# Performance work log

Hardware: AMD Instinct MI355X
Metric: run time of the kernel (lower is better)

Reference implementation:

```python
import jax, jax.numpy as jnp
import numpy as np

EMBED_DIM = 1024
HIDDEN_DIM = 1024
NUM_HEADS = 16
CONTEXT_DIM = 768
HEAD_DIM = EMBED_DIM // NUM_HEADS
SCALE = HEAD_DIM ** -0.5


def setup_inputs() -> dict:
    key = jax.random.key(0)
    ks = jax.random.split(key, 7)
    B, N, M = 4, 4096, 1024
    tokens = jax.random.normal(ks[0], (B, N, HIDDEN_DIM), dtype=jnp.float32)
    context = jax.random.normal(ks[1], (B, M, CONTEXT_DIM), dtype=jnp.float32)
    # Linear weights stored as [in, out] (transposed torch layout)
    Wq = jax.random.normal(ks[2], (HIDDEN_DIM, EMBED_DIM), dtype=jnp.float32) * (HIDDEN_DIM ** -0.5)
    Wk = jax.random.normal(ks[3], (CONTEXT_DIM, EMBED_DIM), dtype=jnp.float32) * (CONTEXT_DIM ** -0.5)
    Wv = jax.random.normal(ks[4], (CONTEXT_DIM, HIDDEN_DIM), dtype=jnp.float32) * (CONTEXT_DIM ** -0.5)
    Wo = jax.random.normal(ks[5], (HIDDEN_DIM, HIDDEN_DIM), dtype=jnp.float32) * (HIDDEN_DIM ** -0.5)
    bo = jax.random.normal(ks[6], (HIDDEN_DIM,), dtype=jnp.float32) * 0.01
    return {"tokens": tokens, "context": context, "Wq": Wq, "Wk": Wk, "Wv": Wv, "Wo": Wo, "bo": bo}


def _split_heads(x):
    # [b, n, h*d] -> [b, h, n, d]
    b, n, _ = x.shape
    return x.reshape(b, n, NUM_HEADS, -1).transpose(0, 2, 1, 3)


def reference(tokens, context, Wq, Wk, Wv, Wo, bo):
    Q = _split_heads(tokens @ Wq)    # [b, h, n, d]
    K = _split_heads(context @ Wk)   # [b, h, m, d]
    V = _split_heads(context @ Wv)   # [b, h, m, dv]
    scores = jnp.einsum('bhnd,bhmd->bhnm', Q, K) * SCALE
    attn = jax.nn.softmax(scores, axis=-1)
    out = jnp.einsum('bhnm,bhmd->bhnd', attn, V)          # [b, h, n, dv]
    b, h, n, d = out.shape
    out = out.transpose(0, 2, 1, 3).reshape(b, n, h * d)  # [b, n, hidden]
    return out @ Wo + bo
```

## Files before the change

### kernel.cpp

```cpp
#include <hip/hip_runtime.h>
#include <hip/hip_bf16.h>
#include <math.h>

typedef unsigned short ushort_t;
typedef __attribute__((ext_vector_type(8))) short short8;
typedef __attribute__((ext_vector_type(4))) short short4v;
typedef __attribute__((ext_vector_type(4))) float f32x4;

#define MFMA16(a, b, c) __builtin_amdgcn_mfma_f32_16x16x32_bf16((a), (b), (c), 0, 0, 0)

__device__ __forceinline__ short8 ld_s8(const void* p) { return *(const short8*)p; }

__device__ __forceinline__ ushort_t f2bf(float x) {
  __hip_bfloat16 h = __float2bfloat16(x);
  return *reinterpret_cast<ushort_t*>(&h);
}

__device__ __forceinline__ void wave_fence() {
  __builtin_amdgcn_fence(__ATOMIC_ACQ_REL, "wavefront");
}

__device__ __forceinline__ void async_ld16(const void* g, void* l) {
  __builtin_amdgcn_global_load_lds(
      (const __attribute__((address_space(1))) unsigned int*)g,
      (__attribute__((address_space(3))) unsigned int*)l, 16, 0, 0);
}

__global__ __launch_bounds__(256) void cvt_k(const float* __restrict__ src,
                                             ushort_t* __restrict__ dst, size_t n8) {
  const size_t i = (size_t)blockIdx.x * 256 + threadIdx.x;
  if (i >= n8) return;
  const size_t base = i * 8;
  const float4 a = ((const float4*)(src + base))[0];
  const float4 b = ((const float4*)(src + base))[1];
  short8 o;
  o[0] = (short)f2bf(a.x); o[1] = (short)f2bf(a.y);
  o[2] = (short)f2bf(a.z); o[3] = (short)f2bf(a.w);
  o[4] = (short)f2bf(b.x); o[5] = (short)f2bf(b.y);
  o[6] = (short)f2bf(b.z); o[7] = (short)f2bf(b.w);
  *(short8*)(dst + base) = o;
}

__global__ void transpose_cvt2_k(const float* __restrict__ s0, const float* __restrict__ s1,
                                 ushort_t* __restrict__ d0, ushort_t* __restrict__ d1,
                                 int R, int C) {
  __shared__ ushort_t tile[32][33];
  const float* src = blockIdx.z ? s1 : s0;
  ushort_t* dst = blockIdx.z ? d1 : d0;
  const int bx = blockIdx.x * 32, by = blockIdx.y * 32;
  const int tx = threadIdx.x, ty = threadIdx.y;
#pragma unroll
  for (int i = 0; i < 32; i += 8)
    tile[ty + i][tx] = f2bf(src[(size_t)(by + ty + i) * C + bx + tx]);
  __syncthreads();
#pragma unroll
  for (int i = 0; i < 32; i += 8)
    dst[(size_t)(bx + ty + i) * R + by + tx] = tile[tx][ty + i];
}

#define BM 128
#define BN 128
#define BK 32

__device__ __forceinline__ void st1(float* p, float v) { *p = v; }
__device__ __forceinline__ void st1(__hip_bfloat16* p, float v) { *p = __float2bfloat16(v); }

__device__ __forceinline__ int2 xcd_swz(int nx) {
  const int id = blockIdx.y * gridDim.x + blockIdx.x;
  const int cpx = (gridDim.x * gridDim.y) >> 3;
  const int nid = (id & 7) * cpx + (id >> 3);
  int2 r; r.x = nid % nx; r.y = nid / nx; return r;
}

#define GSTAGE(sA, sB)                                          \
  do {                                                          \
    async_ld16(Ag + (size_t)srow * K + (k0 + scol), (sA) + wb); \
    async_ld16(Ag + (size_t)(srow + 64) * K + (k0 + scol), (sA) + 2048 + wb); \
    async_ld16(Bg + (size_t)srow * K + (k0 + scol), (sB) + wb); \
    async_ld16(Bg + (size_t)(srow + 64) * K + (k0 + scol), (sB) + 2048 + wb); \
    k0 += BK;                                                   \
  } while (0)

#define GCOMP(sA, sB)                                                     \
  do {                                                                    \
    short8 af[4], bfr[4];                                                 \
    _Pragma("unroll") for (int t = 0; t < 4; ++t) {                       \
      af[t] = ld_s8((sA) + (wm + t * 16 + lr) * BK + quad * 8);           \
      bfr[t] = ld_s8((sB) + (wn + t * 16 + lr) * BK + quad * 8);          \
    }                                                                     \
    _Pragma("unroll") for (int tm = 0; tm < 4; ++tm)                      \
        _Pragma("unroll") for (int tn = 0; tn < 4; ++tn)                  \
            acc[tm][tn] = MFMA16(af[tm], bfr[tn], acc[tm][tn]);           \
  } while (0)

template <typename OutT>
__global__ __launch_bounds__(256) void gemm_bt(const ushort_t* __restrict__ A,
                                               const ushort_t* __restrict__ Bt,
                                               OutT* __restrict__ C,
                                               const float* __restrict__ bias,
                                               int M, int N, int K) {
  __shared__ __align__(16) ushort_t sA0[BM * BK];
  __shared__ __align__(16) ushort_t sA1[BM * BK];
  __shared__ __align__(16) ushort_t sB0[BN * BK];
  __shared__ __align__(16) ushort_t sB1[BN * BK];
  const int tid = threadIdx.x;
  const int lane = tid & 63, wave = tid >> 6;
  const int lr = lane & 15, quad = lane >> 4;
  const int2 bid = xcd_swz(gridDim.x);
  const int m0 = bid.y * BM, n0 = bid.x * BN;
  const int wm = (wave >> 1) * 64, wn = (wave & 1) * 64;
  const ushort_t* Ag = A + (size_t)m0 * K;
  const ushort_t* Bg = Bt + (size_t)n0 * K;
  const int srow = tid >> 2, scol = (tid & 3) * 8;
  const int wb = (tid & 192) * 8;

  f32x4 acc[4][4] = {};
  int k0 = 0;

  GSTAGE(sA0, sB0);
  const int NT2 = K >> 6;
#pragma unroll 1
  for (int i2 = 0; i2 < NT2; ++i2) {
    __syncthreads();
    GSTAGE(sA1, sB1);
    GCOMP(sA0, sB0);
    __syncthreads();
    if (i2 < NT2 - 1) GSTAGE(sA0, sB0);
    GCOMP(sA1, sB1);
  }

#pragma unroll
  for (int tm = 0; tm < 4; ++tm) {
    const int row = m0 + wm + tm * 16 + quad * 4;
#pragma unroll
    for (int tn = 0; tn < 4; ++tn) {
      const int col = n0 + wn + tn * 16 + lr;
      const float bv = bias ? bias[col] : 0.0f;
#pragma unroll
      for (int r = 0; r < 4; ++r)
        st1(&C[(size_t)(row + r) * N + col], acc[tm][tn][r] + bv);
    }
  }
}

__global__ __launch_bounds__(256) void kv_gemm(const ushort_t* __restrict__ A,
                                               const ushort_t* __restrict__ Bt,
                                               ushort_t* __restrict__ KVb,
                                               ushort_t* __restrict__ Vt) {
  const int K = 768;
  __shared__ __align__(16) ushort_t sA0[BM * BK];
  __shared__ __align__(16) ushort_t sA1[BM * BK];
  __shared__ __align__(16) ushort_t sB0[BN * BK];
  __shared__ __align__(16) ushort_t sB1[BN * BK];
  const int tid = threadIdx.x;
  const int lane = tid & 63, wave = tid >> 6;
  const int lr = lane & 15, quad = lane >> 4;
  const int2 bid = xcd_swz(gridDim.x);
  const int m0 = bid.y * BM, n0 = bid.x * BN;
  const int wm = (wave >> 1) * 64, wn = (wave & 1) * 64;
  const ushort_t* Ag = A + (size_t)m0 * K;
  const ushort_t* Bg = Bt + (size_t)n0 * K;
  const int srow = tid >> 2, scol = (tid & 3) * 8;
  const int wb = (tid & 192) * 8;

  f32x4 acc[4][4] = {};
  int k0 = 0;

  GSTAGE(sA0, sB0);
  const int NT2 = K >> 6;
#pragma unroll 1
  for (int i2 = 0; i2 < NT2; ++i2) {
    __syncthreads();
    GSTAGE(sA1, sB1);
    GCOMP(sA0, sB0);
    __syncthreads();
    if (i2 < NT2 - 1) GSTAGE(sA0, sB0);
    GCOMP(sA1, sB1);
  }

#pragma unroll
  for (int tm = 0; tm < 4; ++tm) {
    const int row = m0 + wm + tm * 16 + quad * 4;
    const int b = row >> 10, mloc = row & 1023;
#pragma unroll
    for (int tn = 0; tn < 4; ++tn) {
      const int col = n0 + wn + tn * 16 + lr;
      if (col < 1024) {
#pragma unroll
        for (int r = 0; r < 4; ++r)
          KVb[(size_t)(row + r) * 2048 + col] = f2bf(acc[tm][tn][r]);
      } else {
        ushort_t* vp = Vt + ((size_t)b * 1024 + (col - 1024)) * 1024 + mloc;
#pragma unroll
        for (int r = 0; r < 4; ++r)
          vp[r] = f2bf(acc[tm][tn][r]);
      }
    }
  }
}

__global__ __launch_bounds__(256) void attn_k(const ushort_t* __restrict__ Q,
                                              const ushort_t* __restrict__ KVb,
                                              const ushort_t* __restrict__ Vt,
                                              __hip_bfloat16* __restrict__ O) {
  __shared__ __align__(16) ushort_t sK0[64 * 64];
  __shared__ __align__(16) ushort_t sK1[64 * 64];
  __shared__ __align__(16) ushort_t sV0[64 * 64];
  __shared__ __align__(16) ushort_t sV1[64 * 64];
  __shared__ __align__(16) ushort_t sP[4 * 32 * 64];
  const int tid = threadIdx.x;
  const int lane = tid & 63, wave = tid >> 6;
  const int lr = lane & 15, quad = lane >> 4;
  const int b = blockIdx.z, h = blockIdx.y;
  const int q0 = blockIdx.x * 128 + wave * 32;
  const int key = (lr & 7) << 4;

  const ushort_t* Qg = Q + ((size_t)b * 4096 + q0 + lr) * 1024 + h * 64;
  short8 qf[2][2];
#pragma unroll
  for (int t = 0; t < 2; ++t) {
    qf[t][0] = ld_s8(Qg + (size_t)t * 16 * 1024 + quad * 8);
    qf[t][1] = ld_s8(Qg + (size_t)t * 16 * 1024 + 32 + quad * 8);
  }
  const ushort_t* Kg = KVb + (size_t)b * 1024 * 2048 + h * 64;
  const ushort_t* Vg = Vt + ((size_t)b * 1024 + h * 64) * 1024;

  const int srow = lane >> 3;
  const int scol = ((lane & 7) ^ srow) * 8;
  const ushort_t* k0 = Kg + (size_t)(wave * 8 + srow) * 2048 + scol;
  const ushort_t* v0 = Vg + (size_t)(wave * 8 + srow) * 1024 + scol;
  ushort_t* const dK0 = sK0 + wave * 512;
  ushort_t* const dK1 = sK1 + wave * 512;
  ushort_t* const dV0 = sV0 + wave * 512;
  ushort_t* const dV1 = sV1 + wave * 512;
  ushort_t* const sPw = sP + wave * 2048;

  const float c1 = 0.125f * 1.44269504f;
  const float c2 = 16.0f * 1.44269504f;

  short8 onesb;
#pragma unroll
  for (int i = 0; i < 8; ++i) onesb[i] = (short)0x3F80;

  f32x4 ls0 = {}, ls1 = {};
  f32x4 o0[4] = {}, o1[4] = {};

#define STAGE(dK, dV)                                  \
  do {                                                 \
    async_ld16(k0, (dK));                              \
    async_ld16(k0 + (size_t)32 * 2048, (dK) + 2048);   \
    async_ld16(v0, (dV));                              \
    async_ld16(v0 + (size_t)32 * 1024, (dV) + 2048);   \
    k0 += (size_t)64 * 2048;                           \
    v0 += 64;                                          \
  } while (0)

#define COMPUTE(cK, cV)                                                                   \
  do {                                                                                    \
    _Pragma("unroll") for (int nt = 0; nt < 4; ++nt) {                                    \
      const int krow = nt * 16 + lr;                                                      \
      const short8 ka = ld_s8((const char*)(cK) + ((krow * 128 + quad * 16) ^ key));      \
      const short8 kb = ld_s8((const char*)(cK) + ((krow * 128 + 64 + quad * 16) ^ key)); \
      _Pragma("unroll") for (int t = 0; t < 2; ++t) {                                     \
        f32x4 z = {};                                                                     \
        z = MFMA16(ka, qf[t][0], z);                                                      \
        z = MFMA16(kb, qf[t][1], z);                                                      \
        short4v pk;                                                                       \
        _Pragma("unroll") for (int r = 0; r < 4; ++r) {                                   \
          const float p = __builtin_amdgcn_exp2f(fmaf(z[r], c1, -c2));                    \
          pk[r] = (short)f2bf(p);                                                         \
        }                                                                                 \
        *(short4v*)((char*)sPw + (((t * 16 + lr) * 128 + nt * 32 + quad * 8) ^ key)) = pk;\
      }                                                                                   \
    }                                                                                     \
    wave_fence();                                                                         \
    __builtin_amdgcn_s_setprio(1);                                                        \
    _Pragma("unroll") for (int ks = 0; ks < 2; ++ks) {                                    \
      const short8 p0 = ld_s8((const char*)sPw + ((lr * 128 + ks * 64 + quad * 16) ^ key)); \
      const short8 p1 = ld_s8((const char*)sPw + (((16 + lr) * 128 + ks * 64 + quad * 16) ^ key)); \
      _Pragma("unroll") for (int dt = 0; dt < 4; ++dt) {                                  \
        const short8 vv =                                                                 \
            ld_s8((const char*)(cV) + (((dt * 16 + lr) * 128 + ks * 64 + quad * 16) ^ key)); \
        o0[dt] = MFMA16(p0, vv, o0[dt]);                                                  \
        o1[dt] = MFMA16(p1, vv, o1[dt]);                                                  \
      }                                                                                   \
      ls0 = MFMA16(p0, onesb, ls0);                                                       \
      ls1 = MFMA16(p1, onesb, ls1);                                                       \
    }                                                                                     \
    __builtin_amdgcn_s_setprio(0);                                                        \
    wave_fence();                                                                         \
  } while (0)

  STAGE(dK0, dV0);

#pragma unroll 1
  for (int it2 = 0; it2 < 8; ++it2) {
    __syncthreads();
    STAGE(dK1, dV1);
    COMPUTE(sK0, sV0);
    __syncthreads();
    if (it2 < 7) STAGE(dK0, dV0);
    COMPUTE(sK1, sV1);
  }
#undef STAGE
#undef COMPUTE

#pragma unroll
  for (int t = 0; t < 2; ++t) {
    const f32x4 lt = t ? ls1 : ls0;
    const f32x4* oa = t ? o1 : o0;
    __hip_bfloat16* Og = O + ((size_t)b * 4096 + q0 + t * 16 + quad * 4) * 1024 + h * 64;
#pragma unroll
    for (int r = 0; r < 4; ++r) {
      const float rl = 1.0f / lt[r];
#pragma unroll
      for (int dt = 0; dt < 4; ++dt)
        Og[(size_t)r * 1024 + dt * 16 + lr] = __float2bfloat16(oa[dt][r] * rl);
    }
  }
}

extern "C" void kernel_launch(void* const* d_in, const int* in_sizes, int n_in,
                              void* d_out, int out_size, void* d_ws, size_t ws_size,
                              hipStream_t stream) {
  (void)in_sizes; (void)n_in; (void)out_size; (void)ws_size;
  const float* tokens  = (const float*)d_in[0];
  const float* context = (const float*)d_in[1];
  const float* Wq = (const float*)d_in[2];
  const float* Wk = (const float*)d_in[3];
  const float* Wv = (const float*)d_in[4];
  const float* Wo = (const float*)d_in[5];
  const float* bo = (const float*)d_in[6];
  float* out = (float*)d_out;

  ushort_t* ws = (ushort_t*)d_ws;
  ushort_t* tokB = ws; ws += (size_t)16384 * 1024;
  ushort_t* ctxB = ws; ws += (size_t)4096 * 768;
  ushort_t* WqT  = ws; ws += (size_t)1024 * 1024;
  ushort_t* WkvT = ws; ws += (size_t)2048 * 768;
  ushort_t* WoT  = ws; ws += (size_t)1024 * 1024;
  ushort_t* Qb   = ws; ws += (size_t)16384 * 1024;
  ushort_t* KVb  = ws; ws += (size_t)4096 * 2048;
  ushort_t* Vt   = ws; ws += (size_t)4096 * 1024;
  ushort_t* Ab   = Qb;

  cvt_k<<<8192, 256, 0, stream>>>(tokens, tokB, (size_t)16384 * 1024 / 8);
  cvt_k<<<1536, 256, 0, stream>>>(context, ctxB, (size_t)4096 * 768 / 8);

  const dim3 tb(32, 8);
  transpose_cvt2_k<<<dim3(32, 32, 2), tb, 0, stream>>>(Wq, Wo, WqT, WoT, 1024, 1024);
  transpose_cvt2_k<<<dim3(32, 24, 2), tb, 0, stream>>>(Wk, Wv, WkvT, WkvT + (size_t)1024 * 768,
                                                       768, 1024);

  gemm_bt<__hip_bfloat16><<<dim3(8, 128), 256, 0, stream>>>(
      tokB, WqT, (__hip_bfloat16*)Qb, nullptr, 16384, 1024, 1024);
  kv_gemm<<<dim3(16, 32), 256, 0, stream>>>(ctxB, WkvT, KVb, Vt);

  attn_k<<<dim3(32, 16, 4), 256, 0, stream>>>(Qb, KVb, Vt, (__hip_bfloat16*)Ab);

  gemm_bt<float><<<dim3(8, 128), 256, 0, stream>>>(
      Ab, WoT, out, bo, 16384, 1024, 1024);
}
```

Before: 356.8 us.

## Replace 128x128 GEMM with 256x256 tile, BK=64, XOR-swizzled LDS kernel

Swaps the Q-projection and output-projection GEMMs to a new kernel using 256x256 output tiles per 512-thread block, BK of 64, and an XOR swizzle on the LDS layout to avoid bank conflicts. Larger tiles raise arithmetic intensity and cut redundant global loads. The cost is a grid of only 256 blocks, which may leave some of the GPU's compute units idle. It also uses 128 KB of LDS and more accumulator registers at one block per CU, so less latency can be hidden.

```diff
diff --git a/kernel.cpp b/kernel.cpp
--- a/kernel.cpp
+++ b/kernel.cpp
@@ -58,10 +58,6 @@
     dst[(size_t)(bx + ty + i) * R + by + tx] = tile[tx][ty + i];
 }
 
-#define BM 128
-#define BN 128
-#define BK 32
-
 __device__ __forceinline__ void st1(float* p, float v) { *p = v; }
 __device__ __forceinline__ void st1(__hip_bfloat16* p, float v) { *p = __float2bfloat16(v); }
 
@@ -71,6 +67,89 @@
   const int nid = (id & 7) * cpx + (id >> 3);
   int2 r; r.x = nid % nx; r.y = nid / nx; return r;
 }
+
+#define GSTAGE256(sAx, sBx)                                                        \
+  do {                                                                             \
+    _Pragma("unroll") for (int r0 = 0; r0 < 4; ++r0) {                             \
+      async_ld16(Ag + (size_t)(r0 * 64 + srow) * K + (k0 + scol), (sAx) + r0 * 4096 + wb); \
+      async_ld16(Bg + (size_t)(r0 * 64 + srow) * K + (k0 + scol), (sBx) + r0 * 4096 + wb); \
+    }                                                                              \
+    k0 += 64;                                                                      \
+  } while (0)
+
+#define GCOMP256(sAx, sBx)                                                         \
+  do {                                                                             \
+    _Pragma("unroll") for (int kk = 0; kk < 2; ++kk) {                             \
+      short8 bfr[4];                                                               \
+      _Pragma("unroll") for (int tn = 0; tn < 4; ++tn) {                           \
+        const int rb = wn + tn * 16 + lr;                                          \
+        bfr[tn] = ld_s8((const char*)(sBx) + ((rb * 128 + kk * 64 + quad * 16) ^ key)); \
+      }                                                                            \
+      _Pragma("unroll") for (int tm = 0; tm < 8; ++tm) {                           \
+        const int ra = wm + tm * 16 + lr;                                          \
+        const short8 af = ld_s8((const char*)(sAx) + ((ra * 128 + kk * 64 + quad * 16) ^ key)); \
+        _Pragma("unroll") for (int tn = 0; tn < 4; ++tn)                           \
+          acc[tm][tn] = MFMA16(af, bfr[tn], acc[tm][tn]);                          \
+      }                                                                            \
+    }                                                                              \
+  } while (0)
+
+template <typename OutT>
+__global__ __launch_bounds__(512, 1) void gemm256_bt(const ushort_t* __restrict__ A,
+                                                     const ushort_t* __restrict__ Bt,
+                                                     OutT* __restrict__ C,
+                                                     const float* __restrict__ bias,
+                                                     int M, int N, int K) {
+  __shared__ __align__(16) ushort_t sA0[256 * 64];
+  __shared__ __align__(16) ushort_t sA1[256 * 64];
+  __shared__ __align__(16) ushort_t sB0[256 * 64];
+  __shared__ __align__(16) ushort_t sB1[256 * 64];
+  const int tid = threadIdx.x;
+  const int lane = tid & 63, wave = tid >> 6;
+  const int lr = lane & 15, quad = lane >> 4;
+  const int key = (lr & 7) << 4;
+  const int2 bid = xcd_swz(gridDim.x);
+  const int m0 = bid.y * 256, n0 = bid.x * 256;
+  const int wm = (wave >> 2) * 128;
+  const int wn = (wave & 3) * 64;
+  const ushort_t* Ag = A + (size_t)m0 * K;
+  const ushort_t* Bg = Bt + (size_t)n0 * K;
+  const int srow = tid >> 3;
+  const int scol = ((tid & 7) ^ (srow & 7)) * 8;
+  const int wb = (tid >> 6) * 512;
+
+  f32x4 acc[8][4] = {};
+  int k0 = 0;
+
+  GSTAGE256(sA0, sB0);
+  const int NT2 = K >> 7;
+#pragma unroll 1
+  for (int i2 = 0; i2 < NT2; ++i2) {
+    __syncthreads();
+    GSTAGE256(sA1, sB1);
+    GCOMP256(sA0, sB0);
+    __syncthreads();
+    if (i2 < NT2 - 1) GSTAGE256(sA0, sB0);
+    GCOMP256(sA1, sB1);
+  }
+
+#pragma unroll
+  for (int tm = 0; tm < 8; ++tm) {
+    const int row = m0 + wm + tm * 16 + quad * 4;
+#pragma unroll
+    for (int tn = 0; tn < 4; ++tn) {
+      const int col = n0 + wn + tn * 16 + lr;
+      const float bv = bias ? bias[col] : 0.0f;
+#pragma unroll
+      for (int r = 0; r < 4; ++r)
+        st1(&C[(size_t)(row + r) * N + col], acc[tm][tn][r] + bv);
+    }
+  }
+}
+
+#define BM 128
+#define BN 128
+#define BK 32
 
 #define GSTAGE(sA, sB)                                          \
   do {                                                          \
@@ -92,56 +171,6 @@
         _Pragma("unroll") for (int tn = 0; tn < 4; ++tn)                  \
             acc[tm][tn] = MFMA16(af[tm], bfr[tn], acc[tm][tn]);           \
   } while (0)
-
-template <typename OutT>
-__global__ __launch_bounds__(256) void gemm_bt(const ushort_t* __restrict__ A,
-                                               const ushort_t* __restrict__ Bt,
-                                               OutT* __restrict__ C,
-                                               const float* __restrict__ bias,
-                                               int M, int N, int K) {
-  __shared__ __align__(16) ushort_t sA0[BM * BK];
-  __shared__ __align__(16) ushort_t sA1[BM * BK];
-  __shared__ __align__(16) ushort_t sB0[BN * BK];
-  __shared__ __align__(16) ushort_t sB1[BN * BK];
-  const int tid = threadIdx.x;
-  const int lane = tid & 63, wave = tid >> 6;
-  const int lr = lane & 15, quad = lane >> 4;
-  const int2 bid = xcd_swz(gridDim.x);
-  const int m0 = bid.y * BM, n0 = bid.x * BN;
-  const int wm = (wave >> 1) * 64, wn = (wave & 1) * 64;
-  const ushort_t* Ag = A + (size_t)m0 * K;
-  const ushort_t* Bg = Bt + (size_t)n0 * K;
-  const int srow = tid >> 2, scol = (tid & 3) * 8;
-  const int wb = (tid & 192) * 8;
-
-  f32x4 acc[4][4] = {};
-  int k0 = 0;
-
-  GSTAGE(sA0, sB0);
-  const int NT2 = K >> 6;
-#pragma unroll 1
-  for (int i2 = 0; i2 < NT2; ++i2) {
-    __syncthreads();
-    GSTAGE(sA1, sB1);
-    GCOMP(sA0, sB0);
-    __syncthreads();
-    if (i2 < NT2 - 1) GSTAGE(sA0, sB0);
-    GCOMP(sA1, sB1);
-  }
-
-#pragma unroll
-  for (int tm = 0; tm < 4; ++tm) {
-    const int row = m0 + wm + tm * 16 + quad * 4;
-#pragma unroll
-    for (int tn = 0; tn < 4; ++tn) {
-      const int col = n0 + wn + tn * 16 + lr;
-      const float bv = bias ? bias[col] : 0.0f;
-#pragma unroll
-      for (int r = 0; r < 4; ++r)
-        st1(&C[(size_t)(row + r) * N + col], acc[tm][tn][r] + bv);
-    }
-  }
-}
 
 __global__ __launch_bounds__(256) void kv_gemm(const ushort_t* __restrict__ A,
                                                const ushort_t* __restrict__ Bt,
@@ -352,12 +381,12 @@
   transpose_cvt2_k<<<dim3(32, 24, 2), tb, 0, stream>>>(Wk, Wv, WkvT, WkvT + (size_t)1024 * 768,
                                                        768, 1024);
 
-  gemm_bt<__hip_bfloat16><<<dim3(8, 128), 256, 0, stream>>>(
+  gemm256_bt<__hip_bfloat16><<<dim3(4, 64), 512, 0, stream>>>(
       tokB, WqT, (__hip_bfloat16*)Qb, nullptr, 16384, 1024, 1024);
   kv_gemm<<<dim3(16, 32), 256, 0, stream>>>(ctxB, WkvT, KVb, Vt);
 
   attn_k<<<dim3(32, 16, 4), 256, 0, stream>>>(Qb, KVb, Vt, (__hip_bfloat16*)Ab);
 
-  gemm_bt<float><<<dim3(8, 128), 256, 0, stream>>>(
+  gemm256_bt<float><<<dim3(4, 64), 512, 0, stream>>>(
       Ab, WoT, out, bo, 16384, 1024, 1024);
 }
```

After: 346.5 us. 2.9% less time.
